# Optimization experiments

Hardware: AMD Instinct MI355X
Metric: run time of the kernel (lower is better)

Reference implementation:

```python
import jax, jax.numpy as jnp
import numpy as np

TEMP = 2.0      # softmax temperature
POOL_K = 0.5    # node keep ratio
BN_EPS = 1e-5


def setup_inputs() -> dict:
    key = jax.random.key(0)
    ks = jax.random.split(key, 8)
    bs, n, d = 8, 512, 64
    return {
        "x": jax.random.normal(ks[0], (bs, n, d), jnp.float32),
        "att_w": jax.random.normal(ks[1], (d, d), jnp.float32) / np.sqrt(d),
        "att_b": jnp.zeros((d,), jnp.float32),
        "att_weight": jax.random.normal(ks[2], (d, 1), jnp.float32) / np.sqrt(d),
        "pwa_w": jax.random.normal(ks[3], (d, d), jnp.float32) / np.sqrt(d),
        "pwa_b": jnp.zeros((d,), jnp.float32),
        "pwo_w": jax.random.normal(ks[4], (d, d), jnp.float32) / np.sqrt(d),
        "pwo_b": jnp.zeros((d,), jnp.float32),
        "gamma": jnp.ones((d,), jnp.float32),
        "beta": jnp.zeros((d,), jnp.float32),
        "rmean": jnp.zeros((d,), jnp.float32),
        "rvar": jnp.ones((d,), jnp.float32),
        "pool_w": jax.random.normal(ks[5], (d, 1), jnp.float32) / np.sqrt(d),
        "pool_b": jnp.zeros((1,), jnp.float32),
    }


def reference(x, att_w, att_b, att_weight, pwa_w, pwa_b, pwo_w, pwo_b,
              gamma, beta, rmean, rvar, pool_w, pool_b):
    # --- GraphAttentionLayer (eval mode: dropout = identity) ---
    # pairwise node products: (b, n, n, d)
    pair = x[:, :, None, :] * x[:, None, :, :]
    # tanh(Linear(pair)) then contract with att_weight -> logits (b, n, n)
    t = jnp.tanh(jnp.einsum('bijd,de->bije', pair, att_w) + att_b)
    logits = jnp.einsum('bijd,d->bij', t, att_weight[:, 0]) / TEMP
    # softmax over dim=-2 of (b,n,n,1) == axis 2 here
    attn = jax.nn.softmax(logits, axis=2)           # (b, n, n)
    agg = jnp.einsum('bij,bjd->bid', attn, x)       # attended features
    h = (agg @ pwa_w + pwa_b) + (x @ pwo_w + pwo_b)
    # BatchNorm1d, eval mode over flattened (b*n, d)
    h = (h - rmean) * jax.lax.rsqrt(rvar + BN_EPS) * gamma + beta
    h = jax.nn.selu(h)

    # --- GraphPool (eval mode: dropout = identity) ---
    scores = jax.nn.sigmoid(h @ pool_w + pool_b)    # (b, n, 1)
    n_keep = max(int(h.shape[1] * POOL_K), 1)
    _, idx = jax.lax.top_k(scores[..., 0], n_keep)  # (b, n_keep), desc sorted
    hs = h * scores
    out = jnp.take_along_axis(hs, idx[..., None], axis=1)  # (b, n_keep, d)
    return out
```

## Files before the change

kernel.cpp:

```cpp
#include <hip/hip_runtime.h>

#define NB 8
#define NN 512
#define ND 64
#define NKEEP 256
#define PJ 132
#define WSCALE 2.8853900817779268f
#define K2 0.72134752f

#define SELU_SCALE 1.0507009873554805f
#define SELU_ALPHA 1.6732632423543773f

typedef __attribute__((ext_vector_type(8))) short short8;
typedef __attribute__((ext_vector_type(4))) float f32x4;

__device__ __forceinline__ unsigned short f2bf_rne(float f) {
    unsigned u = __float_as_uint(f);
    return (unsigned short)((u + 0x7fffu + ((u >> 16) & 1u)) >> 16);
}
__device__ __forceinline__ float bf2f(unsigned short h) {
    return __uint_as_float(((unsigned)h) << 16);
}

__device__ __forceinline__ void gl2lds16(const unsigned short* g, unsigned short* l) {
    __builtin_amdgcn_global_load_lds(
        (const __attribute__((address_space(1))) unsigned int*)g,
        (__attribute__((address_space(3))) unsigned int*)l,
        16, 0, 0);
}
__device__ __forceinline__ void gl2lds16f(const float* g, float* l) {
    __builtin_amdgcn_global_load_lds(
        (const __attribute__((address_space(1))) unsigned int*)g,
        (__attribute__((address_space(3))) unsigned int*)l,
        16, 0, 0);
}

__global__ __launch_bounds__(256)
void sast_prep_kernel(const float* __restrict__ x,
                      unsigned short* __restrict__ xh,
                      unsigned short* __restrict__ xl)
{
    int f = blockIdx.x * 256 + threadIdx.x;
    int bb = f >> 13;
    int r  = f & 8191;
    int jg = r >> 4, q = r & 15;
    float4 v = *(const float4*)(x + (bb * NN + jg) * ND + q * 4);
    unsigned short h0 = f2bf_rne(v.x), h1 = f2bf_rne(v.y),
                   h2 = f2bf_rne(v.z), h3 = f2bf_rne(v.w);
    unsigned short l0 = (unsigned short)(__float_as_uint(v.x - bf2f(h0)) >> 16);
    unsigned short l1 = (unsigned short)(__float_as_uint(v.y - bf2f(h1)) >> 16);
    unsigned short l2 = (unsigned short)(__float_as_uint(v.z - bf2f(h2)) >> 16);
    unsigned short l3 = (unsigned short)(__float_as_uint(v.w - bf2f(h3)) >> 16);
    int c = jg >> 7, j = jg & 127;
    int idx = bb * 32768 + c * 8192 + j * 64 + ((q * 4) ^ ((j & 7) << 3));
    *(uint2*)(xh + idx) = make_uint2((unsigned)h0 | ((unsigned)h1 << 16),
                                     (unsigned)h2 | ((unsigned)h3 << 16));
    *(uint2*)(xl + idx) = make_uint2((unsigned)l0 | ((unsigned)l1 << 16),
                                     (unsigned)l2 | ((unsigned)l3 << 16));
}

__global__ __launch_bounds__(512, 4)
void sast_logit_kernel(const float* __restrict__ x,
                       const unsigned short* __restrict__ xh_img,
                       const unsigned short* __restrict__ xl_img,
                       const float* __restrict__ att_w,
                       const float* __restrict__ att_b,
                       const float* __restrict__ att_wt,
                       unsigned short* __restrict__ p_buf)
{
    __shared__ alignas(16) unsigned short Xh[8192];
    __shared__ alignas(16) unsigned short Xl[8192];
    __shared__ float probs[4 * PJ];
    __shared__ float lpP[4 * PJ];
    __shared__ float xg[4 * ND];

    const int tid  = threadIdx.x;
    const int w    = tid >> 6;
    const int iw   = w & 3;
    const int eh   = w >> 2;
    const int lane = tid & 63;
    const int g    = lane >> 4;
    const int rr   = lane & 15;
    const int rnd  = blockIdx.x >> 8;
    const int m0   = blockIdx.x & 31;
    const int m    = (rnd & 1) ? (31 - m0) : m0;
    const int b    = (blockIdx.x >> 5) & 7;
    const int i0   = 128 * rnd + 4 * m;
    const int c0   = rnd;

    const unsigned short* xhb = xh_img + b * 32768;
    const unsigned short* xlb = xl_img + b * 32768;
    unsigned short* pb = p_buf + b * NN * NN;

    float sab = 0.f;
    #pragma unroll
    for (int e4 = 0; e4 < ND; e4 += 4) {
        float4 awv = *(const float4*)(att_wt + e4);
        sab += fabsf(awv.x) + fabsf(awv.y) + fabsf(awv.z) + fabsf(awv.w);
    }
    const float nLam2 = -K2 * sab;

    const int swz = (rr & 7) << 3;
    const int fb0 = rr * 64 + ((g * 8) ^ swz);
    const int fb1 = rr * 64 + ((g * 8 + 32) ^ swz);

    if (tid < 256) xg[tid] = x[(b * NN + i0 + (tid >> 6)) * ND + (tid & 63)];
    __syncthreads();

    {
        const int base = w * 1024;
        gl2lds16(xhb + c0 * 8192 + base +       (lane << 3), &Xh[base]);
        gl2lds16(xhb + c0 * 8192 + base + 512 + (lane << 3), &Xh[base + 512]);
        gl2lds16(xlb + c0 * 8192 + base +       (lane << 3), &Xl[base]);
        gl2lds16(xlb + c0 * 8192 + base + 512 + (lane << 3), &Xl[base + 512]);
    }

    short8 Wh[2][2], Wl[2][2];
    #pragma unroll
    for (int mt2 = 0; mt2 < 2; ++mt2) {
        const int mt = eh * 2 + mt2;
        #pragma unroll
        for (int ks = 0; ks < 2; ++ks) {
            #pragma unroll
            for (int t = 0; t < 8; ++t) {
                int d = ks * 32 + g * 8 + t;
                int e = mt * 16 + rr;
                float wv = att_w[d * ND + e] * xg[iw * ND + d] * WSCALE;
                unsigned short hh = f2bf_rne(wv);
                unsigned short ll = (unsigned short)(__float_as_uint(wv - bf2f(hh)) >> 16);
                Wh[mt2][ks][t] = (short)hh;
                Wl[mt2][ks][t] = (short)ll;
            }
        }
    }
    f32x4 attb4[2], mw4[2];
    float basep = 0.f;
    #pragma unroll
    for (int mt2 = 0; mt2 < 2; ++mt2) {
        const int mt = eh * 2 + mt2;
        #pragma unroll
        for (int r = 0; r < 4; ++r) {
            int e = mt * 16 + g * 4 + r;
            float aw = att_wt[e];
            attb4[mt2][r] = att_b[e] * WSCALE;
            mw4[mt2][r]   = -2.0f * aw;
            basep += aw;
        }
    }
    __syncthreads();

    for (int c = c0; c < 4; ++c) {
        if (c != c0) {
            const int base = w * 1024;
            gl2lds16(xhb + c * 8192 + base +       (lane << 3), &Xh[base]);
            gl2lds16(xhb + c * 8192 + base + 512 + (lane << 3), &Xh[base + 512]);
            gl2lds16(xlb + c * 8192 + base +       (lane << 3), &Xl[base]);
            gl2lds16(xlb + c * 8192 + base + 512 + (lane << 3), &Xl[base + 512]);
            __syncthreads();
        }
        const int jb = c << 7;
        const int jt0 = (i0 > jb) ? ((i0 - jb) >> 4) : 0;

        float lp_own[8];
        #pragma unroll
        for (int jt = jt0; jt < 8; ++jt) {
            short8 bh0 = *(const short8*)(Xh + fb0 + jt * 1024);
            short8 bh1 = *(const short8*)(Xh + fb1 + jt * 1024);
            short8 bl0 = *(const short8*)(Xl + fb0 + jt * 1024);
            short8 bl1 = *(const short8*)(Xl + fb1 + jt * 1024);
            float lp = basep;
            #pragma unroll
            for (int mt2 = 0; mt2 < 2; ++mt2) {
                f32x4 acc = attb4[mt2];
                acc = __builtin_amdgcn_mfma_f32_16x16x32_bf16(Wh[mt2][0], bh0, acc, 0, 0, 0);
                acc = __builtin_amdgcn_mfma_f32_16x16x32_bf16(Wh[mt2][1], bh1, acc, 0, 0, 0);
                acc = __builtin_amdgcn_mfma_f32_16x16x32_bf16(Wh[mt2][0], bl0, acc, 0, 0, 0);
                acc = __builtin_amdgcn_mfma_f32_16x16x32_bf16(Wh[mt2][1], bl1, acc, 0, 0, 0);
                acc = __builtin_amdgcn_mfma_f32_16x16x32_bf16(Wl[mt2][0], bh0, acc, 0, 0, 0);
                acc = __builtin_amdgcn_mfma_f32_16x16x32_bf16(Wl[mt2][1], bh1, acc, 0, 0, 0);
                f32x4 mw = mw4[mt2];
                float u0 = exp2f(fminf(acc[0], 60.f));
                float u1 = exp2f(fminf(acc[1], 60.f));
                float u2 = exp2f(fminf(acc[2], 60.f));
                float u3 = exp2f(fminf(acc[3], 60.f));
                float n01 = fmaf(mw[0], u1, fmaf(mw[1], u0, mw[0] + mw[1]));
                float d01 = fmaf(u0, u1, 1.0f + (u0 + u1));
                float n23 = fmaf(mw[2], u3, fmaf(mw[3], u2, mw[2] + mw[3]));
                float d23 = fmaf(u2, u3, 1.0f + (u2 + u3));
                lp = fmaf(n01, __builtin_amdgcn_rcpf(d01), lp);
                lp = fmaf(n23, __builtin_amdgcn_rcpf(d23), lp);
            }
            lp += __shfl_xor(lp, 16);
            lp += __shfl_xor(lp, 32);
            if (eh == 0) lp_own[jt] = lp;
            else if (lane < 16) lpP[iw * PJ + jt * 16 + rr] = lp;
        }
        __syncthreads();

        if (eh == 0 && lane < 16) {
            #pragma unroll
            for (int jt = jt0; jt < 8; ++jt) {
                float t = lp_own[jt] + lpP[iw * PJ + jt * 16 + rr];
                probs[iw * PJ + jt * 16 + rr] = exp2f(fmaf(t, K2, nLam2));
            }
        }
        __syncthreads();

        {
            const int iw2 = tid >> 7, jl = tid & 127, j = jb + jl;
            if (j >= i0) {
                float p = fminf(probs[iw2 * PJ + jl], 1.0f);
                pb[(i0 + iw2) * NN + j] =
                    (unsigned short)__float2uint_rn(p * 65535.f);
            }
        }
    }
}

__global__ __launch_bounds__(512, 4)
void sast_agg_kernel(const float* __restrict__ x,
                     const unsigned short* __restrict__ p_buf,
                     const float* __restrict__ pwa_w,
                     const float* __restrict__ pwa_b,
                     const float* __restrict__ pwo_w,
                     const float* __restrict__ pwo_b,
                     const float* __restrict__ gma,
                     const float* __restrict__ bta,
                     const float* __restrict__ rmean,
                     const float* __restrict__ rvar,
                     const float* __restrict__ pool_w,
                     const float* __restrict__ pool_b,
                     float* __restrict__ ws_h,
                     float* __restrict__ ws_score)
{
    __shared__ alignas(16) float Xc[8192];
    __shared__ alignas(16) unsigned short prow[4096];
    __shared__ alignas(16) unsigned short pcolT[4096];
    __shared__ float xrow[8 * ND];
    __shared__ float aggsh[8 * ND];

    const int tid  = threadIdx.x;
    const int w    = tid >> 6;
    const int lane = tid & 63;
    const int b    = blockIdx.x >> 6;
    const int i0   = (blockIdx.x & 63) * 8;
    const int i    = i0 + w;
    const float* xb = x + b * NN * ND;
    const unsigned short* pbb = p_buf + b * NN * NN;

    gl2lds16(pbb + (i0 + w) * NN + (lane << 3), &prow[w << 9]);
    if (tid < i0 + 4)
        *(uint4*)(&pcolT[tid * 8]) = *(const uint4*)(pbb + tid * NN + i0);
    #pragma unroll
    for (int r = 0; r < 4; ++r)
        gl2lds16f(xb + w * 1024 + r * 256 + (lane << 2), &Xc[w * 1024 + r * 256]);
    xrow[w * ND + lane] = xb[i * ND + lane];
    __syncthreads();

    const int B = i0 + ((w >= 4) ? 4 : 0);
    for (int j = lane; j < B; j += 64)
        prow[(w << 9) + j] = pcolT[j * 8 + w];

    uint4 q = *(const uint4*)(&prow[(w << 9) + (lane << 3)]);
    unsigned us = (q.x & 0xffffu) + (q.x >> 16) + (q.y & 0xffffu) + (q.y >> 16)
                + (q.z & 0xffffu) + (q.z >> 16) + (q.w & 0xffffu) + (q.w >> 16);
    #pragma unroll
    for (int m = 32; m; m >>= 1) us += (unsigned)__shfl_xor((int)us, m);
    const float Sinv = __fdividef(1.0f, (float)us);

    float acc = 0.f;
    for (int c = 0; c < 4; ++c) {
        if (c) {
            __syncthreads();
            #pragma unroll
            for (int r = 0; r < 4; ++r)
                gl2lds16f(xb + c * 8192 + w * 1024 + r * 256 + (lane << 2),
                          &Xc[w * 1024 + r * 256]);
            __syncthreads();
        }
        const int jb = c << 7;
        #pragma unroll 4
        for (int jl = 0; jl < 128; jl += 2) {
            unsigned pu = *(const unsigned*)(&prow[(w << 9) + jb + jl]);
            acc = fmaf((float)(pu & 0xffffu), Xc[jl * 64 + lane], acc);
            acc = fmaf((float)(pu >> 16),     Xc[(jl + 1) * 64 + lane], acc);
        }
    }
    aggsh[w * ND + lane] = acc * Sinv;

    float hv = pwa_b[lane] + pwo_b[lane];
    #pragma unroll 4
    for (int d = 0; d < ND; ++d)
        hv = fmaf(aggsh[w * ND + d], pwa_w[d * ND + lane],
             fmaf(xrow[w * ND + d], pwo_w[d * ND + lane], hv));
    hv = (hv - rmean[lane]) * rsqrtf(rvar[lane] + 1e-5f) * gma[lane] + bta[lane];
    hv = hv > 0.f ? SELU_SCALE * hv
                  : SELU_SCALE * SELU_ALPHA * (__expf(hv) - 1.0f);
    ws_h[(b * NN + i) * ND + lane] = hv;
    float sc = hv * pool_w[lane];
    #pragma unroll
    for (int m = 32; m; m >>= 1) sc += __shfl_xor(sc, m);
    if (lane == 0)
        ws_score[b * NN + i] = __fdividef(1.0f, 1.0f + __expf(-(sc + pool_b[0])));
}

__global__ void sast_topk_kernel(const float* __restrict__ ws_h,
                                 const float* __restrict__ ws_score,
                                 float* __restrict__ out)
{
    __shared__ float s[NN];
    __shared__ int sel[NKEEP];
    const int b = blockIdx.x, tid = threadIdx.x;
    s[tid] = ws_score[b * NN + tid];
    __syncthreads();
    const float v = s[tid];
    int rank = 0;
    for (int j = 0; j < NN; ++j) {
        float sj = s[j];
        rank += ((sj > v) || (sj == v && j < tid)) ? 1 : 0;
    }
    if (rank < NKEEP) sel[rank] = tid;
    __syncthreads();
    #pragma unroll
    for (int it = 0; it < NKEEP * ND / 512; ++it) {
        int f = it * 512 + tid;
        int k = f >> 6, e = f & 63;
        int j = sel[k];
        out[(b * NKEEP + k) * ND + e] = ws_h[(b * NN + j) * ND + e] * s[j];
    }
}

extern "C" void kernel_launch(void* const* d_in, const int* in_sizes, int n_in,
                              void* d_out, int out_size, void* d_ws, size_t ws_size,
                              hipStream_t stream)
{
    const float* x      = (const float*)d_in[0];
    const float* att_w  = (const float*)d_in[1];
    const float* att_b  = (const float*)d_in[2];
    const float* att_wt = (const float*)d_in[3];
    const float* pwa_w  = (const float*)d_in[4];
    const float* pwa_b  = (const float*)d_in[5];
    const float* pwo_w  = (const float*)d_in[6];
    const float* pwo_b  = (const float*)d_in[7];
    const float* gma    = (const float*)d_in[8];
    const float* bta    = (const float*)d_in[9];
    const float* rmean  = (const float*)d_in[10];
    const float* rvar   = (const float*)d_in[11];
    const float* pool_w = (const float*)d_in[12];
    const float* pool_b = (const float*)d_in[13];
    float* out   = (float*)d_out;
    float* ws_h  = (float*)d_ws;
    float* ws_sc = ws_h + NB * NN * ND;
    unsigned short* xh_img = (unsigned short*)(ws_sc + NB * NN);
    unsigned short* xl_img = xh_img + NB * NN * ND;
    unsigned short* p_buf  = xl_img + NB * NN * ND;

    sast_prep_kernel<<<256, 256, 0, stream>>>(x, xh_img, xl_img);
    sast_logit_kernel<<<NB * 128, 512, 0, stream>>>(
        x, xh_img, xl_img, att_w, att_b, att_wt, p_buf);
    sast_agg_kernel<<<NB * 64, 512, 0, stream>>>(
        x, p_buf, pwa_w, pwa_b, pwo_w, pwo_b,
        gma, bta, rmean, rvar, pool_w, pool_b, ws_h, ws_sc);
    sast_topk_kernel<<<NB, 512, 0, stream>>>(ws_h, ws_sc, out);
}
```

Measured before the change: 92.38 us.

## Prefetch next X chunk early in logit kernel; widen agg blocks to 16 rows

In the logit kernel, the load of the next column chunk of the bf16 x images now starts right after the logit barrier. It overlaps with the probability and exp stores instead of sitting before the next compute phase, which also removes one barrier per chunk. The aggregation kernel now runs 16 rows per block with 1024 threads, so each staged X chunk is reused by twice as many rows. Its inner accumulation is split into two independent FMA chains. The trade-off is more LDS per block and fewer blocks (256), which may hurt occupancy and latency hiding.

```diff
diff --git a/kernel.cpp b/kernel.cpp
--- a/kernel.cpp
+++ b/kernel.cpp
@@ -150,14 +150,6 @@
     __syncthreads();
 
     for (int c = c0; c < 4; ++c) {
-        if (c != c0) {
-            const int base = w * 1024;
-            gl2lds16(xhb + c * 8192 + base +       (lane << 3), &Xh[base]);
-            gl2lds16(xhb + c * 8192 + base + 512 + (lane << 3), &Xh[base + 512]);
-            gl2lds16(xlb + c * 8192 + base +       (lane << 3), &Xl[base]);
-            gl2lds16(xlb + c * 8192 + base + 512 + (lane << 3), &Xl[base + 512]);
-            __syncthreads();
-        }
         const int jb = c << 7;
         const int jt0 = (i0 > jb) ? ((i0 - jb) >> 4) : 0;
 
@@ -197,6 +189,14 @@
         }
         __syncthreads();
 
+        if (c < 3) {
+            const int base = w * 1024;
+            gl2lds16(xhb + (c + 1) * 8192 + base +       (lane << 3), &Xh[base]);
+            gl2lds16(xhb + (c + 1) * 8192 + base + 512 + (lane << 3), &Xh[base + 512]);
+            gl2lds16(xlb + (c + 1) * 8192 + base +       (lane << 3), &Xl[base]);
+            gl2lds16(xlb + (c + 1) * 8192 + base + 512 + (lane << 3), &Xl[base + 512]);
+        }
+
         if (eh == 0 && lane < 16) {
             #pragma unroll
             for (int jt = jt0; jt < 8; ++jt) {
@@ -217,7 +217,7 @@
     }
 }
 
-__global__ __launch_bounds__(512, 4)
+__global__ __launch_bounds__(1024, 2)
 void sast_agg_kernel(const float* __restrict__ x,
                      const unsigned short* __restrict__ p_buf,
                      const float* __restrict__ pwa_w,
@@ -234,32 +234,33 @@
                      float* __restrict__ ws_score)
 {
     __shared__ alignas(16) float Xc[8192];
-    __shared__ alignas(16) unsigned short prow[4096];
-    __shared__ alignas(16) unsigned short pcolT[4096];
-    __shared__ float xrow[8 * ND];
-    __shared__ float aggsh[8 * ND];
+    __shared__ alignas(16) unsigned short prow[16 * NN];
+    __shared__ alignas(16) unsigned short pcolT[NN * 16];
+    __shared__ float xrow[16 * ND];
+    __shared__ float aggsh[16 * ND];
 
     const int tid  = threadIdx.x;
     const int w    = tid >> 6;
     const int lane = tid & 63;
-    const int b    = blockIdx.x >> 6;
-    const int i0   = (blockIdx.x & 63) * 8;
+    const int b    = blockIdx.x >> 5;
+    const int i0   = (blockIdx.x & 31) * 16;
     const int i    = i0 + w;
     const float* xb = x + b * NN * ND;
     const unsigned short* pbb = p_buf + b * NN * NN;
 
-    gl2lds16(pbb + (i0 + w) * NN + (lane << 3), &prow[w << 9]);
-    if (tid < i0 + 4)
-        *(uint4*)(&pcolT[tid * 8]) = *(const uint4*)(pbb + tid * NN + i0);
-    #pragma unroll
-    for (int r = 0; r < 4; ++r)
-        gl2lds16f(xb + w * 1024 + r * 256 + (lane << 2), &Xc[w * 1024 + r * 256]);
-    xrow[w * ND + lane] = xb[i * ND + lane];
-    __syncthreads();
-
-    const int B = i0 + ((w >= 4) ? 4 : 0);
+    gl2lds16(pbb + i * NN + (lane << 3), &prow[w << 9]);
+    gl2lds16f(xb + w * 512 +       (lane << 2), &Xc[w * 512]);
+    gl2lds16f(xb + w * 512 + 256 + (lane << 2), &Xc[w * 512 + 256]);
+    for (int t = tid; t < i0 + 12; t += 1024) {
+        *(uint4*)(&pcolT[t * 16])     = *(const uint4*)(pbb + t * NN + i0);
+        *(uint4*)(&pcolT[t * 16 + 8]) = *(const uint4*)(pbb + t * NN + i0 + 8);
+    }
+    xrow[tid] = xb[i0 * ND + tid];
+    __syncthreads();
+
+    const int B = i0 + (w & ~3);
     for (int j = lane; j < B; j += 64)
-        prow[(w << 9) + j] = pcolT[j * 8 + w];
+        prow[(w << 9) + j] = pcolT[j * 16 + w];
 
     uint4 q = *(const uint4*)(&prow[(w << 9) + (lane << 3)]);
     unsigned us = (q.x & 0xffffu) + (q.x >> 16) + (q.y & 0xffffu) + (q.y >> 16)
@@ -268,25 +269,23 @@
     for (int m = 32; m; m >>= 1) us += (unsigned)__shfl_xor((int)us, m);
     const float Sinv = __fdividef(1.0f, (float)us);
 
-    float acc = 0.f;
+    float acc0 = 0.f, acc1 = 0.f;
     for (int c = 0; c < 4; ++c) {
         if (c) {
             __syncthreads();
-            #pragma unroll
-            for (int r = 0; r < 4; ++r)
-                gl2lds16f(xb + c * 8192 + w * 1024 + r * 256 + (lane << 2),
-                          &Xc[w * 1024 + r * 256]);
+            gl2lds16f(xb + c * 8192 + w * 512 +       (lane << 2), &Xc[w * 512]);
+            gl2lds16f(xb + c * 8192 + w * 512 + 256 + (lane << 2), &Xc[w * 512 + 256]);
             __syncthreads();
         }
         const int jb = c << 7;
         #pragma unroll 4
         for (int jl = 0; jl < 128; jl += 2) {
             unsigned pu = *(const unsigned*)(&prow[(w << 9) + jb + jl]);
-            acc = fmaf((float)(pu & 0xffffu), Xc[jl * 64 + lane], acc);
-            acc = fmaf((float)(pu >> 16),     Xc[(jl + 1) * 64 + lane], acc);
-        }
-    }
-    aggsh[w * ND + lane] = acc * Sinv;
+            acc0 = fmaf((float)(pu & 0xffffu), Xc[jl * 64 + lane], acc0);
+            acc1 = fmaf((float)(pu >> 16),     Xc[(jl + 1) * 64 + lane], acc1);
+        }
+    }
+    aggsh[w * ND + lane] = (acc0 + acc1) * Sinv;
 
     float hv = pwa_b[lane] + pwo_b[lane];
     #pragma unroll 4
@@ -358,7 +357,7 @@
     sast_prep_kernel<<<256, 256, 0, stream>>>(x, xh_img, xl_img);
     sast_logit_kernel<<<NB * 128, 512, 0, stream>>>(
         x, xh_img, xl_img, att_w, att_b, att_wt, p_buf);
-    sast_agg_kernel<<<NB * 64, 512, 0, stream>>>(
+    sast_agg_kernel<<<NB * 32, 1024, 0, stream>>>(
         x, p_buf, pwa_w, pwa_b, pwo_w, pwo_b,
         gma, bta, rmean, rvar, pool_w, pool_b, ws_h, ws_sc);
     sast_topk_kernel<<<NB, 512, 0, stream>>>(ws_h, ws_sc, out);
```

New measurement: 92.67 us. Within noise of the previous version (+0.3%).
